# Performance work log

Hardware: AMD Instinct MI355X
Metric: run time of the kernel (lower is better)

Reference implementation:

```python
import jax, jax.numpy as jnp
import numpy as np

N_NODES = 100000
N_EDGES = 640000
IN_DIM = 128
OUT_DIM = 128
EDGE_DIM = 4
N_GROUPS = 8
EPS = 1e-5


def setup_inputs() -> dict:
    key = jax.random.key(0)
    ks = jax.random.split(key, 9)
    x = jax.random.normal(ks[0], (N_NODES, IN_DIM), dtype=jnp.float32)
    edge_index = jax.random.randint(ks[1], (2, N_EDGES), 0, N_NODES, dtype=jnp.int64)
    edge_attr = jax.random.normal(ks[2], (N_EDGES, EDGE_DIM), dtype=jnp.float32)
    d_in = 2 * IN_DIM + EDGE_DIM
    # Linear layers (kaiming-uniform-ish init scale)
    W1 = jax.random.uniform(ks[3], (d_in, OUT_DIM), jnp.float32, -1, 1) / np.sqrt(d_in)
    b1 = jax.random.uniform(ks[4], (OUT_DIM,), jnp.float32, -1, 1) / np.sqrt(d_in)
    W2 = jax.random.uniform(ks[5], (OUT_DIM, OUT_DIM), jnp.float32, -1, 1) / np.sqrt(OUT_DIM)
    b2 = jax.random.uniform(ks[6], (OUT_DIM,), jnp.float32, -1, 1) / np.sqrt(OUT_DIM)
    gn_gamma = jnp.ones((OUT_DIM,), jnp.float32)
    gn_beta = jnp.zeros((OUT_DIM,), jnp.float32)
    return {"x": x, "edge_index": edge_index, "edge_attr": edge_attr,
            "W1": W1, "b1": b1, "gn_gamma": gn_gamma, "gn_beta": gn_beta,
            "W2": W2, "b2": b2}


def group_norm(h, gamma, beta):
    # h: [E, C]; normalize each row per group of C//N_GROUPS channels
    E, C = h.shape
    hg = h.reshape(E, N_GROUPS, C // N_GROUPS)
    mean = jnp.mean(hg, axis=-1, keepdims=True)
    var = jnp.mean(jnp.square(hg - mean), axis=-1, keepdims=True)
    hg = (hg - mean) * jax.lax.rsqrt(var + EPS)
    return hg.reshape(E, C) * gamma + beta


def reference(x, edge_index, edge_attr, W1, b1, gn_gamma, gn_beta, W2, b2):
    src, dst = edge_index[0], edge_index[1]
    # gather endpoint features: [E, 2*in_dim + edge_dim]
    feat = jnp.concatenate([x[dst], x[src], edge_attr], axis=-1)
    h = feat @ W1 + b1                      # [E, out_dim]
    h = group_norm(h, gn_gamma, gn_beta)
    h = jax.nn.silu(h)
    messages = h @ W2 + b2                  # [E, out_dim]
    out = jax.ops.segment_sum(messages, dst, num_segments=x.shape[0])
    count = jax.ops.segment_sum(jnp.ones((messages.shape[0], 1), x.dtype), dst,
                                num_segments=x.shape[0])
    return out / jnp.maximum(count, 1.0)
```

## Files before the change

### kernel.cpp

```cpp
#include <hip/hip_runtime.h>
#include <hip/hip_bf16.h>

#define NNODES 100000
#define NEDGES 640000
#define DIM 128
#define GS 16
#define EB 64
#define NSCAN_BLOCKS ((NNODES + 255) / 256)
#define G1_BLOCKS ((NNODES + 63) / 64)

typedef __attribute__((ext_vector_type(8))) short short8;
typedef __attribute__((ext_vector_type(4))) float f32x4;

__device__ __forceinline__ ushort f2bf(float f) {
    __hip_bfloat16 h = __float2bfloat16(f);
    return *reinterpret_cast<ushort*>(&h);
}
__device__ __forceinline__ float bf2f(ushort u) {
    union { unsigned int i; float f; } v; v.i = ((unsigned int)u) << 16; return v.f;
}

__global__ void zero_kernel(float* __restrict__ out, int* __restrict__ hist) {
    long step = (long)gridDim.x * blockDim.x;
    long i0 = (long)blockIdx.x * blockDim.x + threadIdx.x;
    const long total = (long)NNODES * DIM;
    for (long i = i0; i < total; i += step) out[i] = 0.f;
    for (long i = i0; i < NNODES; i += step) hist[i] = 0;
}

__global__ __launch_bounds__(256) void node_gemm1(const float* __restrict__ x,
                                                  const float* __restrict__ W1,
                                                  const float* __restrict__ b1,
                                                  ushort* __restrict__ xab) {
    __shared__ __align__(16) char xt[64 * 256];
    const int tid  = threadIdx.x;
    const int lane = tid & 63;
    const int w    = tid >> 6;
    const int lr   = lane & 15;
    const int lg   = lane >> 4;
    const int m0   = blockIdx.x * 64;
    const int mtMax = (m0 + 64 <= NNODES) ? 4 : 2;

    const int koff = (w >= 2) ? 128 : 0;
    short8 bfrag[4][4];
    #pragma unroll
    for (int nt = 0; nt < 4; ++nt) {
        const int cc = (w & 1) * 64 + nt * 16 + lr;
        #pragma unroll
        for (int kt = 0; kt < 4; ++kt) {
            const int kb = koff + kt * 32 + lg * 8;
            short8 f;
            #pragma unroll
            for (int j = 0; j < 8; ++j) f[j] = (short)f2bf(W1[(long)(kb + j) * DIM + cc]);
            bfrag[nt][kt] = f;
        }
    }

    {
        const int r  = tid >> 2;
        const int kq = (tid & 3) * 32;
        if (m0 + r < NNODES) {
            const float* xr = &x[(long)(m0 + r) * DIM + kq];
            ushort tmp[32];
            #pragma unroll
            for (int j = 0; j < 32; ++j) tmp[j] = f2bf(xr[j]);
            #pragma unroll
            for (int i = 0; i < 4; ++i) {
                int byte = r * 256 + kq * 2 + i * 16;
                byte ^= (r & 7) << 4;
                *(short8*)(xt + byte) = *(short8*)&tmp[i * 8];
            }
        }
    }
    __syncthreads();

    const int colBase = w * 64;
    for (int mt = 0; mt < mtMax; ++mt) {
        short8 afrag[4];
        #pragma unroll
        for (int kt = 0; kt < 4; ++kt) {
            const int row = mt * 16 + lr;
            int byte = row * 256 + (kt * 4 + lg) * 16;
            byte ^= (row & 7) << 4;
            afrag[kt] = *(short8*)(xt + byte);
        }
        f32x4 acc[4] = {};
        #pragma unroll
        for (int nt = 0; nt < 4; ++nt)
            #pragma unroll
            for (int kt = 0; kt < 4; ++kt)
                acc[nt] = __builtin_amdgcn_mfma_f32_16x16x32_bf16(afrag[kt], bfrag[nt][kt], acc[nt], 0, 0, 0);
        #pragma unroll
        for (int nt = 0; nt < 4; ++nt) {
            const int col = colBase + nt * 16 + lr;
            const float badd = (koff == 0) ? b1[col] : 0.f;
            #pragma unroll
            for (int r = 0; r < 4; ++r) {
                const int row = m0 + mt * 16 + lg * 4 + r;
                xab[(long)row * 256 + col] = f2bf(acc[nt][r] + badd);
            }
        }
    }
}

__global__ void hist_kernel(const int* __restrict__ ei, int* __restrict__ hist) {
    int e = blockIdx.x * 256 + threadIdx.x;
    if (e < NEDGES) atomicAdd(&hist[ei[NEDGES + e]], 1);
}

__global__ void scan1_kernel(const int* __restrict__ hist, int* __restrict__ excl,
                             int* __restrict__ bsums) {
    __shared__ int s[256];
    int tid = threadIdx.x;
    int i = blockIdx.x * 256 + tid;
    int v = (i < NNODES) ? hist[i] : 0;
    s[tid] = v;
    __syncthreads();
    for (int o = 1; o < 256; o <<= 1) {
        int t = (tid >= o) ? s[tid - o] : 0;
        __syncthreads();
        s[tid] += t;
        __syncthreads();
    }
    if (i < NNODES) excl[i] = s[tid] - v;
    if (tid == 255) bsums[blockIdx.x] = s[255];
}

__global__ void scan2_kernel(int* __restrict__ bsums) {
    __shared__ int s[512];
    int tid = threadIdx.x;
    int v = (tid < NSCAN_BLOCKS) ? bsums[tid] : 0;
    s[tid] = v;
    __syncthreads();
    for (int o = 1; o < 512; o <<= 1) {
        int t = (tid >= o) ? s[tid - o] : 0;
        __syncthreads();
        s[tid] += t;
        __syncthreads();
    }
    if (tid < NSCAN_BLOCKS) bsums[tid] = s[tid] - v;
}

__global__ void scan3_kernel(const int* __restrict__ excl, const int* __restrict__ bsums,
                             int* __restrict__ cursor) {
    int i = blockIdx.x * 256 + threadIdx.x;
    if (i < NNODES) cursor[i] = excl[i] + bsums[blockIdx.x];
}

__global__ void scatter_kernel(const int* __restrict__ ei, const float* __restrict__ ea,
                               int* __restrict__ cursor,
                               int2* __restrict__ dstsrc, float4* __restrict__ eas) {
    int e = blockIdx.x * 256 + threadIdx.x;
    if (e < NEDGES) {
        int d = ei[NEDGES + e];
        int pos = atomicAdd(&cursor[d], 1);
        dstsrc[pos] = make_int2(d, ei[e]);
        eas[pos] = *(const float4*)&ea[(long)e * 4];
    }
}

__global__ __launch_bounds__(256) void edge_silu_kernel(
    const ushort* __restrict__ xab,
    const int2* __restrict__ dstsrc, const float4* __restrict__ eas,
    const float* __restrict__ W1,
    const float* __restrict__ gamma, const float* __restrict__ beta,
    float* __restrict__ out)
{
    __shared__ __align__(16) ushort ssilu[EB * 128];
    __shared__ __align__(16) float4 w1ct[132];
    __shared__ __align__(8)  float2 gbt[132];
    __shared__ int2   sds[EB];
    __shared__ float4 sea4[EB];

    const int tid = threadIdx.x;
    const int e0 = blockIdx.x * EB;

    if (tid < EB) {
        sds[tid]  = dstsrc[e0 + tid];
        sea4[tid] = eas[e0 + tid];
    }
    if (tid < 128) {
        int c = tid;
        int p = c + (c >> 5);
        w1ct[p] = make_float4(W1[256 * DIM + c], W1[257 * DIM + c],
                              W1[258 * DIM + c], W1[259 * DIM + c]);
        gbt[p] = make_float2(gamma[c], beta[c]);
    }
    __syncthreads();

    {
        const int e = tid >> 2;
        const int q = tid & 3;
        const int c0 = q * 32;
        const int pBase = c0 + q;
        const int2 ds = sds[e];
        const ushort* xaRow = &xab[(long)ds.x * 256 + c0];
        const ushort* xbRow = &xab[(long)ds.y * 256 + 128 + c0];
        const float4 a = sea4[e];

        float v[32];
        #pragma unroll
        for (int i = 0; i < 4; ++i) {
            short8 ga = *(const short8*)&xaRow[i * 8];
            short8 gb = *(const short8*)&xbRow[i * 8];
            #pragma unroll
            for (int j = 0; j < 8; ++j) {
                const int idx = i * 8 + j;
                const float4 w = w1ct[pBase + idx];
                float t = a.x * w.x + a.y * w.y;
                t += a.z * w.z + a.w * w.w;
                v[idx] = t + bf2f((ushort)ga[j]) + bf2f((ushort)gb[j]);
            }
        }

        #pragma unroll
        for (int g = 0; g < 2; ++g) {
            float s = 0.f, qq = 0.f;
            #pragma unroll
            for (int i = 0; i < GS; ++i) {
                float a2 = v[g * GS + i];
                s += a2; qq += a2 * a2;
            }
            const float m = s * (1.f / GS);
            const float var = qq * (1.f / GS) - m * m;
            const float inv = __builtin_amdgcn_rsqf(var + 1e-5f);
            #pragma unroll
            for (int i = 0; i < GS; ++i) {
                const int idx = g * GS + i;
                const float2 gb2 = gbt[pBase + idx];
                const float sc = gb2.x * inv;
                const float off = gb2.y - m * sc;
                float t = v[idx] * sc + off;
                v[idx] = t * __builtin_amdgcn_rcpf(1.f + __expf(-t));
            }
        }

        ushort tmp[32];
        #pragma unroll
        for (int j = 0; j < 32; ++j) tmp[j] = f2bf(v[j]);
        #pragma unroll
        for (int i = 0; i < 4; ++i) {
            int byte = (e * 256 + (c0 + i * 8) * 2) ^ ((e & 7) << 4);
            *(short8*)((char*)ssilu + byte) = *(short8*)&tmp[i * 8];
        }
    }
    __syncthreads();

    {
        const int c = tid & 127;
        const int h = tid >> 7;
        const int eS = h * 32, eE = eS + 32;
        float r = 0.f;
        int cur = sds[eS].x;
        for (int ee = eS; ee < eE; ++ee) {
            int d = sds[ee].x;
            if (d != cur) {
                unsafeAtomicAdd(&out[(long)cur * DIM + c], r);
                r = 0.f; cur = d;
            }
            int byte = (ee * 256 + c * 2) ^ ((ee & 7) << 4);
            r += bf2f(*(const ushort*)((const char*)ssilu + byte));
        }
        unsafeAtomicAdd(&out[(long)cur * DIM + c], r);
    }
}

__global__ __launch_bounds__(256) void node_gemm2(float* __restrict__ out,
                                                  const float* __restrict__ W2,
                                                  const float* __restrict__ b2,
                                                  const int* __restrict__ hist) {
    __shared__ __align__(16) char at[64 * 256];
    __shared__ float sb2[128];
    __shared__ int scnt[64];
    const int tid  = threadIdx.x;
    const int lane = tid & 63;
    const int w    = tid >> 6;
    const int lr   = lane & 15;
    const int lg   = lane >> 4;
    const int m0   = blockIdx.x * 64;
    const int mtMax = (m0 + 64 <= NNODES) ? 4 : 2;

    short8 bfrag[2][4];
    #pragma unroll
    for (int nt = 0; nt < 2; ++nt) {
        const int cc = w * 32 + nt * 16 + lr;
        #pragma unroll
        for (int kt = 0; kt < 4; ++kt) {
            const int kb = kt * 32 + lg * 8;
            short8 f;
            #pragma unroll
            for (int j = 0; j < 8; ++j) f[j] = (short)f2bf(W2[(long)(kb + j) * DIM + cc]);
            bfrag[nt][kt] = f;
        }
    }

    if (tid < 128) sb2[tid] = b2[tid];
    if (tid < 64 && m0 + tid < NNODES) scnt[tid] = hist[m0 + tid];

    {
        const int r  = tid >> 2;
        const int kq = (tid & 3) * 32;
        if (m0 + r < NNODES) {
            const float* ar = &out[(long)(m0 + r) * DIM + kq];
            ushort tmp[32];
            #pragma unroll
            for (int j = 0; j < 32; ++j) tmp[j] = f2bf(ar[j]);
            #pragma unroll
            for (int i = 0; i < 4; ++i) {
                int byte = r * 256 + kq * 2 + i * 16;
                byte ^= (r & 7) << 4;
                *(short8*)(at + byte) = *(short8*)&tmp[i * 8];
            }
        }
    }
    __syncthreads();

    for (int mt = 0; mt < mtMax; ++mt) {
        short8 afrag[4];
        #pragma unroll
        for (int kt = 0; kt < 4; ++kt) {
            const int row = mt * 16 + lr;
            int byte = row * 256 + (kt * 4 + lg) * 16;
            byte ^= (row & 7) << 4;
            afrag[kt] = *(short8*)(at + byte);
        }
        f32x4 acc[2] = {};
        #pragma unroll
        for (int nt = 0; nt < 2; ++nt)
            #pragma unroll
            for (int kt = 0; kt < 4; ++kt)
                acc[nt] = __builtin_amdgcn_mfma_f32_16x16x32_bf16(afrag[kt], bfrag[nt][kt], acc[nt], 0, 0, 0);
        #pragma unroll
        for (int nt = 0; nt < 2; ++nt) {
            const int col = w * 32 + nt * 16 + lr;
            #pragma unroll
            for (int r = 0; r < 4; ++r) {
                const int rr = mt * 16 + lg * 4 + r;
                float cnt = (float)scnt[rr];
                float sc = __builtin_amdgcn_rcpf(fmaxf(cnt, 1.f));
                out[(long)(m0 + rr) * DIM + col] = (acc[nt][r] + cnt * sb2[col]) * sc;
            }
        }
    }
}

extern "C" void kernel_launch(void* const* d_in, const int* in_sizes, int n_in,
                              void* d_out, int out_size, void* d_ws, size_t ws_size,
                              hipStream_t stream) {
    const float* x     = (const float*)d_in[0];
    const int*   ei    = (const int*)  d_in[1];
    const float* ea    = (const float*)d_in[2];
    const float* W1    = (const float*)d_in[3];
    const float* b1    = (const float*)d_in[4];
    const float* gamma = (const float*)d_in[5];
    const float* beta  = (const float*)d_in[6];
    const float* W2    = (const float*)d_in[7];
    const float* b2    = (const float*)d_in[8];
    float* out = (float*)d_out;

    char* ws = (char*)d_ws;
    size_t off = 0;
    ushort* xab   = (ushort*)(ws + off); off += (size_t)NNODES * 256 * sizeof(ushort);
    int*    hist  = (int*)   (ws + off); off += (size_t)NNODES * sizeof(int);
    int*    excl  = (int*)   (ws + off); off += (size_t)NNODES * sizeof(int);
    int*    cursor= (int*)   (ws + off); off += (size_t)NNODES * sizeof(int);
    int*    bsums = (int*)   (ws + off); off += 512 * sizeof(int);
    int2*   dstsrc= (int2*)  (ws + off); off += (size_t)NEDGES * sizeof(int2);
    off = (off + 15) & ~(size_t)15;
    float4* eas   = (float4*)(ws + off); off += (size_t)NEDGES * sizeof(float4);

    zero_kernel<<<2048, 256, 0, stream>>>(out, hist);
    node_gemm1<<<G1_BLOCKS, 256, 0, stream>>>(x, W1, b1, xab);
    hist_kernel<<<(NEDGES + 255) / 256, 256, 0, stream>>>(ei, hist);
    scan1_kernel<<<NSCAN_BLOCKS, 256, 0, stream>>>(hist, excl, bsums);
    scan2_kernel<<<1, 512, 0, stream>>>(bsums);
    scan3_kernel<<<NSCAN_BLOCKS, 256, 0, stream>>>(excl, bsums, cursor);
    scatter_kernel<<<(NEDGES + 255) / 256, 256, 0, stream>>>(ei, ea, cursor, dstsrc, eas);
    edge_silu_kernel<<<NEDGES / EB, 256, 0, stream>>>(xab, dstsrc, eas,
                                                      W1, gamma, beta, out);
    node_gemm2<<<G1_BLOCKS, 256, 0, stream>>>(out, W2, b2, hist);
}
```

Measured before the change: 215.3 us.

## Prepack weights once, fold scan3 into scatter, vectorize edge GN/SiLU with float2

Adds a pack kernel that converts W1 and W2 to bf16 once, already laid out as MFMA fragments, so each GEMM block loads short8 vectors instead of doing strided scalar gathers and conversions. Removes the scan3 kernel: scatter now computes each position from the exclusive scan plus the block sum plus a per-node atomic counter, at the cost of zeroing an extra counter array. The edge kernel is rewritten to work on channel pairs with float2 vector math and packed bf16 unpacking, with the weight, gamma and beta tables repacked into float4 pairs. This trades one kernel launch for another and adds two extra loads per edge in scatter.

```diff
diff --git a/kernel.cpp b/kernel.cpp
--- a/kernel.cpp
+++ b/kernel.cpp
@@ -11,6 +11,8 @@
 
 typedef __attribute__((ext_vector_type(8))) short short8;
 typedef __attribute__((ext_vector_type(4))) float f32x4;
+typedef __attribute__((ext_vector_type(2))) float f2;
+typedef __attribute__((ext_vector_type(4))) unsigned int uint4v;
 
 __device__ __forceinline__ ushort f2bf(float f) {
     __hip_bfloat16 h = __float2bfloat16(f);
@@ -19,17 +21,47 @@
 __device__ __forceinline__ float bf2f(ushort u) {
     union { unsigned int i; float f; } v; v.i = ((unsigned int)u) << 16; return v.f;
 }
-
-__global__ void zero_kernel(float* __restrict__ out, int* __restrict__ hist) {
+__device__ __forceinline__ f2 sp(float x) { return (f2){x, x}; }
+
+__global__ void zero_kernel(float* __restrict__ out, int* __restrict__ hist,
+                            int* __restrict__ cnt) {
     long step = (long)gridDim.x * blockDim.x;
     long i0 = (long)blockIdx.x * blockDim.x + threadIdx.x;
     const long total = (long)NNODES * DIM;
     for (long i = i0; i < total; i += step) out[i] = 0.f;
-    for (long i = i0; i < NNODES; i += step) hist[i] = 0;
+    for (long i = i0; i < NNODES; i += step) { hist[i] = 0; cnt[i] = 0; }
+}
+
+__global__ void pack_w_kernel(const float* __restrict__ W1, const float* __restrict__ W2,
+                              ushort* __restrict__ w1p, ushort* __restrict__ w2p) {
+    int idx = blockIdx.x * 256 + threadIdx.x;
+    if (idx < 32768) {
+        int j    = idx & 7;
+        int lane = (idx >> 3) & 63;
+        int kt   = (idx >> 9) & 3;
+        int nt   = (idx >> 11) & 3;
+        int w    = (idx >> 13) & 3;
+        int lr = lane & 15, lg = lane >> 4;
+        int koff = (w >= 2) ? 128 : 0;
+        int cc = (w & 1) * 64 + nt * 16 + lr;
+        int kb = koff + kt * 32 + lg * 8;
+        w1p[idx] = f2bf(W1[(long)(kb + j) * DIM + cc]);
+    } else {
+        int i2 = idx - 32768;
+        int j    = i2 & 7;
+        int lane = (i2 >> 3) & 63;
+        int kt   = (i2 >> 9) & 3;
+        int nt   = (i2 >> 11) & 1;
+        int w    = (i2 >> 12) & 3;
+        int lr = lane & 15, lg = lane >> 4;
+        int cc = w * 32 + nt * 16 + lr;
+        int kb = kt * 32 + lg * 8;
+        w2p[i2] = f2bf(W2[(long)(kb + j) * DIM + cc]);
+    }
 }
 
 __global__ __launch_bounds__(256) void node_gemm1(const float* __restrict__ x,
-                                                  const float* __restrict__ W1,
+                                                  const ushort* __restrict__ w1p,
                                                   const float* __restrict__ b1,
                                                   ushort* __restrict__ xab) {
     __shared__ __align__(16) char xt[64 * 256];
@@ -40,21 +72,14 @@
     const int lg   = lane >> 4;
     const int m0   = blockIdx.x * 64;
     const int mtMax = (m0 + 64 <= NNODES) ? 4 : 2;
-
     const int koff = (w >= 2) ? 128 : 0;
+
     short8 bfrag[4][4];
     #pragma unroll
-    for (int nt = 0; nt < 4; ++nt) {
-        const int cc = (w & 1) * 64 + nt * 16 + lr;
-        #pragma unroll
-        for (int kt = 0; kt < 4; ++kt) {
-            const int kb = koff + kt * 32 + lg * 8;
-            short8 f;
-            #pragma unroll
-            for (int j = 0; j < 8; ++j) f[j] = (short)f2bf(W1[(long)(kb + j) * DIM + cc]);
-            bfrag[nt][kt] = f;
-        }
-    }
+    for (int nt = 0; nt < 4; ++nt)
+        #pragma unroll
+        for (int kt = 0; kt < 4; ++kt)
+            bfrag[nt][kt] = *(const short8*)&w1p[(((w * 4 + nt) * 4 + kt) << 9) + lane * 8];
 
     {
         const int r  = tid >> 2;
@@ -141,19 +166,14 @@
     if (tid < NSCAN_BLOCKS) bsums[tid] = s[tid] - v;
 }
 
-__global__ void scan3_kernel(const int* __restrict__ excl, const int* __restrict__ bsums,
-                             int* __restrict__ cursor) {
-    int i = blockIdx.x * 256 + threadIdx.x;
-    if (i < NNODES) cursor[i] = excl[i] + bsums[blockIdx.x];
-}
-
 __global__ void scatter_kernel(const int* __restrict__ ei, const float* __restrict__ ea,
-                               int* __restrict__ cursor,
+                               const int* __restrict__ excl, const int* __restrict__ bsums,
+                               int* __restrict__ cnt,
                                int2* __restrict__ dstsrc, float4* __restrict__ eas) {
     int e = blockIdx.x * 256 + threadIdx.x;
     if (e < NEDGES) {
         int d = ei[NEDGES + e];
-        int pos = atomicAdd(&cursor[d], 1);
+        int pos = excl[d] + bsums[d >> 8] + atomicAdd(&cnt[d], 1);
         dstsrc[pos] = make_int2(d, ei[e]);
         eas[pos] = *(const float4*)&ea[(long)e * 4];
     }
@@ -167,8 +187,9 @@
     float* __restrict__ out)
 {
     __shared__ __align__(16) ushort ssilu[EB * 128];
-    __shared__ __align__(16) float4 w1ct[132];
-    __shared__ __align__(8)  float2 gbt[132];
+    __shared__ __align__(16) float4 wA[68];
+    __shared__ __align__(16) float4 wB[68];
+    __shared__ __align__(16) float4 gbp[68];
     __shared__ int2   sds[EB];
     __shared__ float4 sea4[EB];
 
@@ -178,13 +199,16 @@
     if (tid < EB) {
         sds[tid]  = dstsrc[e0 + tid];
         sea4[tid] = eas[e0 + tid];
-    }
-    if (tid < 128) {
-        int c = tid;
-        int p = c + (c >> 5);
-        w1ct[p] = make_float4(W1[256 * DIM + c], W1[257 * DIM + c],
-                              W1[258 * DIM + c], W1[259 * DIM + c]);
-        gbt[p] = make_float2(gamma[c], beta[c]);
+        if (tid < 64) {
+            int pi = tid;
+            int c0 = 2 * pi;
+            int p = pi + (pi >> 4);
+            wA[p]  = make_float4(W1[256 * DIM + c0], W1[256 * DIM + c0 + 1],
+                                 W1[257 * DIM + c0], W1[257 * DIM + c0 + 1]);
+            wB[p]  = make_float4(W1[258 * DIM + c0], W1[258 * DIM + c0 + 1],
+                                 W1[259 * DIM + c0], W1[259 * DIM + c0 + 1]);
+            gbp[p] = make_float4(gamma[c0], gamma[c0 + 1], beta[c0], beta[c0 + 1]);
+        }
     }
     __syncthreads();
 
@@ -192,52 +216,64 @@
         const int e = tid >> 2;
         const int q = tid & 3;
         const int c0 = q * 32;
-        const int pBase = c0 + q;
         const int2 ds = sds[e];
-        const ushort* xaRow = &xab[(long)ds.x * 256 + c0];
-        const ushort* xbRow = &xab[(long)ds.y * 256 + 128 + c0];
+        const uint* xaRow = (const uint*)&xab[(long)ds.x * 256 + c0];
+        const uint* xbRow = (const uint*)&xab[(long)ds.y * 256 + 128 + c0];
         const float4 a = sea4[e];
 
-        float v[32];
+        uint4v ua[4], ub[4];
         #pragma unroll
         for (int i = 0; i < 4; ++i) {
-            short8 ga = *(const short8*)&xaRow[i * 8];
-            short8 gb = *(const short8*)&xbRow[i * 8];
-            #pragma unroll
-            for (int j = 0; j < 8; ++j) {
-                const int idx = i * 8 + j;
-                const float4 w = w1ct[pBase + idx];
-                float t = a.x * w.x + a.y * w.y;
-                t += a.z * w.z + a.w * w.w;
-                v[idx] = t + bf2f((ushort)ga[j]) + bf2f((ushort)gb[j]);
-            }
+            ua[i] = *(const uint4v*)&xaRow[i * 4];
+            ub[i] = *(const uint4v*)&xbRow[i * 4];
+        }
+
+        f2 v2[16];
+        #pragma unroll
+        for (int k = 0; k < 16; ++k) {
+            const int p = q * 16 + k + q;
+            const float4 a01 = wA[p];
+            const float4 a23 = wB[p];
+            f2 acc = (f2){a01.x, a01.y} * sp(a.x) + (f2){a01.z, a01.w} * sp(a.y)
+                   + (f2){a23.x, a23.y} * sp(a.z) + (f2){a23.z, a23.w} * sp(a.w);
+            const uint uga = ua[k >> 2][k & 3];
+            const uint ugb = ub[k >> 2][k & 3];
+            acc += (f2){__uint_as_float(uga << 16), __uint_as_float(uga & 0xffff0000u)};
+            acc += (f2){__uint_as_float(ugb << 16), __uint_as_float(ugb & 0xffff0000u)};
+            v2[k] = acc;
         }
 
         #pragma unroll
         for (int g = 0; g < 2; ++g) {
-            float s = 0.f, qq = 0.f;
-            #pragma unroll
-            for (int i = 0; i < GS; ++i) {
-                float a2 = v[g * GS + i];
-                s += a2; qq += a2 * a2;
-            }
-            const float m = s * (1.f / GS);
-            const float var = qq * (1.f / GS) - m * m;
+            f2 s = sp(0.f), ss = sp(0.f);
+            #pragma unroll
+            for (int ip = 0; ip < 8; ++ip) {
+                f2 a2 = v2[g * 8 + ip];
+                s += a2; ss += a2 * a2;
+            }
+            const float sum = s.x + s.y;
+            const float sq  = ss.x + ss.y;
+            const float m = sum * (1.f / GS);
+            const float var = sq * (1.f / GS) - m * m;
             const float inv = __builtin_amdgcn_rsqf(var + 1e-5f);
             #pragma unroll
-            for (int i = 0; i < GS; ++i) {
-                const int idx = g * GS + i;
-                const float2 gb2 = gbt[pBase + idx];
-                const float sc = gb2.x * inv;
-                const float off = gb2.y - m * sc;
-                float t = v[idx] * sc + off;
-                v[idx] = t * __builtin_amdgcn_rcpf(1.f + __expf(-t));
+            for (int ip = 0; ip < 8; ++ip) {
+                const int k = g * 8 + ip;
+                const int p = q * 16 + k + q;
+                const float4 gb4 = gbp[p];
+                f2 sc  = (f2){gb4.x, gb4.y} * sp(inv);
+                f2 off = (f2){gb4.z, gb4.w} - sc * sp(m);
+                f2 t = v2[k] * sc + off;
+                f2 r;
+                r.x = t.x * __builtin_amdgcn_rcpf(1.f + __expf(-t.x));
+                r.y = t.y * __builtin_amdgcn_rcpf(1.f + __expf(-t.y));
+                v2[k] = r;
             }
         }
 
         ushort tmp[32];
         #pragma unroll
-        for (int j = 0; j < 32; ++j) tmp[j] = f2bf(v[j]);
+        for (int k = 0; k < 16; ++k) { tmp[2 * k] = f2bf(v2[k].x); tmp[2 * k + 1] = f2bf(v2[k].y); }
         #pragma unroll
         for (int i = 0; i < 4; ++i) {
             int byte = (e * 256 + (c0 + i * 8) * 2) ^ ((e & 7) << 4);
@@ -266,7 +302,7 @@
 }
 
 __global__ __launch_bounds__(256) void node_gemm2(float* __restrict__ out,
-                                                  const float* __restrict__ W2,
+                                                  const ushort* __restrict__ w2p,
                                                   const float* __restrict__ b2,
                                                   const int* __restrict__ hist) {
     __shared__ __align__(16) char at[64 * 256];
@@ -282,17 +318,10 @@
 
     short8 bfrag[2][4];
     #pragma unroll
-    for (int nt = 0; nt < 2; ++nt) {
-        const int cc = w * 32 + nt * 16 + lr;
-        #pragma unroll
-        for (int kt = 0; kt < 4; ++kt) {
-            const int kb = kt * 32 + lg * 8;
-            short8 f;
-            #pragma unroll
-            for (int j = 0; j < 8; ++j) f[j] = (short)f2bf(W2[(long)(kb + j) * DIM + cc]);
-            bfrag[nt][kt] = f;
-        }
-    }
+    for (int nt = 0; nt < 2; ++nt)
+        #pragma unroll
+        for (int kt = 0; kt < 4; ++kt)
+            bfrag[nt][kt] = *(const short8*)&w2p[(((w * 2 + nt) * 4 + kt) << 9) + lane * 8];
 
     if (tid < 128) sb2[tid] = b2[tid];
     if (tid < 64 && m0 + tid < NNODES) scnt[tid] = hist[m0 + tid];
@@ -363,20 +392,23 @@
     ushort* xab   = (ushort*)(ws + off); off += (size_t)NNODES * 256 * sizeof(ushort);
     int*    hist  = (int*)   (ws + off); off += (size_t)NNODES * sizeof(int);
     int*    excl  = (int*)   (ws + off); off += (size_t)NNODES * sizeof(int);
-    int*    cursor= (int*)   (ws + off); off += (size_t)NNODES * sizeof(int);
+    int*    cnt   = (int*)   (ws + off); off += (size_t)NNODES * sizeof(int);
     int*    bsums = (int*)   (ws + off); off += 512 * sizeof(int);
     int2*   dstsrc= (int2*)  (ws + off); off += (size_t)NEDGES * sizeof(int2);
     off = (off + 15) & ~(size_t)15;
     float4* eas   = (float4*)(ws + off); off += (size_t)NEDGES * sizeof(float4);
-
-    zero_kernel<<<2048, 256, 0, stream>>>(out, hist);
-    node_gemm1<<<G1_BLOCKS, 256, 0, stream>>>(x, W1, b1, xab);
+    ushort* w1p   = (ushort*)(ws + off); off += 32768 * sizeof(ushort);
+    ushort* w2p   = (ushort*)(ws + off); off += 16384 * sizeof(ushort);
+
+    zero_kernel<<<2048, 256, 0, stream>>>(out, hist, cnt);
+    pack_w_kernel<<<192, 256, 0, stream>>>(W1, W2, w1p, w2p);
+    node_gemm1<<<G1_BLOCKS, 256, 0, stream>>>(x, w1p, b1, xab);
     hist_kernel<<<(NEDGES + 255) / 256, 256, 0, stream>>>(ei, hist);
     scan1_kernel<<<NSCAN_BLOCKS, 256, 0, stream>>>(hist, excl, bsums);
     scan2_kernel<<<1, 512, 0, stream>>>(bsums);
-    scan3_kernel<<<NSCAN_BLOCKS, 256, 0, stream>>>(excl, bsums, cursor);
-    scatter_kernel<<<(NEDGES + 255) / 256, 256, 0, stream>>>(ei, ea, cursor, dstsrc, eas);
+    scatter_kernel<<<(NEDGES + 255) / 256, 256, 0, stream>>>(ei, ea, excl, bsums, cnt,
+                                                             dstsrc, eas);
     edge_silu_kernel<<<NEDGES / EB, 256, 0, stream>>>(xab, dstsrc, eas,
                                                       W1, gamma, beta, out);
-    node_gemm2<<<G1_BLOCKS, 256, 0, stream>>>(out, W2, b2, hist);
-}
+    node_gemm2<<<G1_BLOCKS, 256, 0, stream>>>(out, w2p, b2, hist);
+}
```

Result: faster. 193.4 us (-10.2%).
